# Performance work log

Hardware: AMD Instinct MI355X
Metric: run time of the kernel (lower is better)

## Reference

```python
import jax, jax.numpy as jnp
import numpy as np

NBINS = 29
NODES = 5


def setup_inputs() -> dict:
    key = jax.random.key(0)
    ks = jax.random.split(key, 9)
    B, Tq, Td, V, H = 64, 32, 4096, 100000, 300
    sentence = jax.random.randint(ks[0], (B, Td), 0, V)
    query_sentence = jax.random.randint(ks[1], (B, Tq), 0, V)
    query_idf = jax.random.uniform(ks[2], (B, Tq), jnp.float32)
    emb = jax.random.normal(ks[3], (V, H), jnp.float32)
    w1 = jax.random.uniform(ks[4], (NBINS + 1, NODES), jnp.float32, -0.1, 0.1)
    b1 = jnp.zeros((NODES,), jnp.float32)
    w2 = jax.random.uniform(ks[5], (NODES, 1), jnp.float32, -0.1, 0.1)
    b2 = jnp.zeros((1,), jnp.float32)
    gate_w = jax.random.uniform(ks[6], (1,), jnp.float32, -0.01, 0.01)
    out_w = jax.random.normal(ks[7], (1, 1), jnp.float32) * 0.1
    out_b = jnp.zeros((1,), jnp.float32)
    return dict(sentence=sentence, query_sentence=query_sentence, query_idf=query_idf,
                emb=emb, w1=w1, b1=b1, w2=w2, b2=b2, gate_w=gate_w, out_w=out_w, out_b=out_b)


def reference(sentence, query_sentence, query_idf, emb, w1, b1, w2, b2, gate_w, out_w, out_b):
    B, Td = sentence.shape
    Tq = query_sentence.shape[1]
    q_mask = (query_sentence != 0).astype(jnp.float32)  # (B,Tq)
    d_mask = (sentence != 0).astype(jnp.float32)        # (B,Td)
    qx = emb[query_sentence]                            # (B,Tq,H)
    dx = emb[sentence]                                  # (B,Td,H)
    q_norm = jnp.sqrt(jnp.sum(qx * qx, -1) + 1e-7)[:, :, None] + 1e-7
    d_norm = jnp.sqrt(jnp.sum(dx * dx, -1) + 1e-7)[:, None, :] + 1e-7
    sim = jnp.einsum('bqh,bdh->bqd', qx, dx) / q_norm / d_norm  # (B,Tq,Td)
    sim = sim + (1.0 - d_mask)[:, None, :] * 1e7  # push masked doc positions out of all bins
    # Histogram: original does nbins cumulative (sim < ub) passes then a cumulative
    # subtraction; equivalent per-element bin index + one scatter-add pass.
    ubs = jnp.linspace(-1.0, 1.0, NBINS + 1)[1:]
    idx = jnp.searchsorted(ubs, sim, side='right')  # bin j <=> ub[j-1] <= sim < ub[j]; NBINS = out-of-range
    rows = jnp.arange(B * Tq)[:, None]
    counts = jnp.zeros((B * Tq, NBINS), jnp.float32).at[rows, idx.reshape(B * Tq, Td)].add(1.0, mode='drop')
    counts = counts.reshape(B, Tq, NBINS)
    exact = jnp.sum((sim > 0.999) & (sim < 1.001), axis=-1).astype(jnp.float32)  # exact-match bin
    hist = jnp.log(jnp.concatenate([counts, exact[..., None]], axis=-1) + 1.0)   # histType == 'LCH'
    ffw = jnp.tanh(jnp.tanh(hist @ w1 + b1) @ w2 + b2)[..., 0]  # (B,Tq)
    # gateType == 'IDF': Linear(1,1,bias=False) on idf, masked softmax over query terms
    gate_logits = query_idf * gate_w[0] + (1.0 - q_mask) * -1e7
    w = jax.nn.softmax(gate_logits, axis=1)
    x = jnp.sum(w * ffw, axis=-1, keepdims=True)  # (B,1)
    return x * out_w[0, 0] + out_b
```

## Files before the change

kernel.cpp:

```cpp
#include <hip/hip_runtime.h>
#include <hip/hip_bf16.h>
#include <math.h>

#define B_    64
#define TQ    32
#define TD    4096
#define HDIM  300
#define NB    29
#define NFEAT 30
#define NKT   19
#define THREADS 256
#define NCH   2
#define DPB   128
#define RDEP  8
#define QF_SLOTS (NKT * 2 * 64)
#define QF_F4    (QF_SLOTS / 2)
#define QF_BYTES (QF_SLOTS * 8)

typedef _Float16 half4 __attribute__((ext_vector_type(4)));
typedef float    f32x4 __attribute__((ext_vector_type(4)));

__device__ __forceinline__ float ubf(int k) {
    return (float)(-1.0 + (2.0 * (double)(k + 1)) / 29.0);
}

__device__ __forceinline__ void bin_one(float sim, unsigned* s_hist, int q) {
    if (sim > 0.999f && sim < 1.001f) {
        atomicAdd(&s_hist[q * NFEAT + 28], 1u);
        atomicAdd(&s_hist[q * NFEAT + 29], 1u);
    } else {
        int idx = (int)((sim + 1.0f) * 14.5f);
        idx = idx < 0 ? 0 : (idx > NB ? NB : idx);
        while (idx < NB && sim >= ubf(idx)) ++idx;
        while (idx > 0 && sim < ubf(idx - 1)) --idx;
        if (idx < NB) atomicAdd(&s_hist[q * NFEAT + idx], 1u);
    }
}

__global__ void k_qfrag(const int* __restrict__ qsent, const float* __restrict__ emb,
                        _Float16* __restrict__ qf, float* __restrict__ invq,
                        unsigned* __restrict__ ghist) {
    const int b = blockIdx.x;
    const int t = threadIdx.x;
    const int row = t & 31, seg = t >> 5;
    __shared__ float pn[8][TQ];
    for (int i = t; i < TQ * NFEAT; i += 256) ghist[b * TQ * NFEAT + i] = 0u;
    const int tok = qsent[b * TQ + row];
    const float* p = emb + (size_t)tok * HDIM;
    _Float16* qfb = qf + (size_t)b * (QF_SLOTS * 4);
    float n = 0.f;
#pragma unroll
    for (int i = 0; i < 10; ++i) {
        const int jf = seg * 10 + i;
        if (jf < 76) {
            const int kg = jf * 4;
            float4 v = make_float4(0.f, 0.f, 0.f, 0.f);
            if (kg < 297) v = *(const float4*)(p + kg);
            n = fmaf(v.x, v.x, n); n = fmaf(v.y, v.y, n);
            n = fmaf(v.z, v.z, n); n = fmaf(v.w, v.w, n);
            half4 h = {(_Float16)v.x, (_Float16)v.y, (_Float16)v.z, (_Float16)v.w};
            const int kt = jf >> 2, g = jf & 3;
            const int slot = (kt * 2 + (row >> 4)) * 64 + (row & 15) + 16 * g;
            *(half4*)&qfb[slot * 4] = h;
        }
    }
    pn[seg][row] = n;
    __syncthreads();
    if (t < TQ) {
        float s = ((pn[0][t] + pn[1][t]) + (pn[2][t] + pn[3][t]))
                + ((pn[4][t] + pn[5][t]) + (pn[6][t] + pn[7][t]));
        invq[b * TQ + t] = 1.0f / (sqrtf(s + 1e-7f) + 1e-7f);
    }
}

__global__ __launch_bounds__(THREADS) void k_main(
        const int* __restrict__ sent, const float* __restrict__ emb,
        const _Float16* __restrict__ qf, const float* __restrict__ invq,
        unsigned* __restrict__ ghist) {
    __shared__ __align__(16) _Float16 afr[QF_SLOTS * 4];
    __shared__ float    s_iq[TQ];
    __shared__ unsigned s_hist[TQ * NFEAT];

    const int b    = blockIdx.x >> 5;
    const int d0   = (blockIdx.x & 31) * DPB;
    const int tid  = threadIdx.x;
    const int wid  = tid >> 6;
    const int lane = tid & 63;

    const int g4   = lane >> 4;
    const int r16  = lane & 15;

    int tok[NCH];
    const float* bp[NCH];
#pragma unroll
    for (int ch = 0; ch < NCH; ++ch) {
        tok[ch] = sent[b * TD + d0 + ch * 64 + wid * 16 + r16];
        bp[ch]  = emb + (size_t)tok[ch] * HDIM + g4 * 4;
    }

    auto ldBg = [&](int g) -> float4 {
        const int ch = g / NKT, kt = g - ch * NKT;
        if (kt == 18 && g4 == 3) return make_float4(0.f, 0.f, 0.f, 0.f);
        return *(const float4*)(bp[ch] + kt * 16);
    };

    float4 pre[RDEP];
#pragma unroll
    for (int p = 0; p < RDEP; ++p) pre[p] = ldBg(p);

    for (int i = tid; i < TQ * NFEAT; i += THREADS) s_hist[i] = 0u;
    {
        const float4* qfp = (const float4*)(qf + (size_t)b * (QF_SLOTS * 4));
        float4* afp = (float4*)afr;
        for (int i = tid; i < QF_F4; i += THREADS) afp[i] = qfp[i];
    }
    if (tid < TQ) s_iq[tid] = invq[b * TQ + tid];
    __syncthreads();

#pragma unroll
    for (int ch = 0; ch < NCH; ++ch) {
        f32x4 acc0 = {0.f, 0.f, 0.f, 0.f};
        f32x4 acc1 = {0.f, 0.f, 0.f, 0.f};
        float nd = 0.f;
#pragma unroll
        for (int kt = 0; kt < NKT; ++kt) {
            const int g = ch * NKT + kt;
            float4 v = pre[g % RDEP];
            if (g + RDEP < NCH * NKT) pre[g % RDEP] = ldBg(g + RDEP);
            nd = fmaf(v.x, v.x, nd); nd = fmaf(v.y, v.y, nd);
            nd = fmaf(v.z, v.z, nd); nd = fmaf(v.w, v.w, nd);
            half4 hb = {(_Float16)v.x, (_Float16)v.y, (_Float16)v.z, (_Float16)v.w};
            half4 a0 = *(const half4*)&afr[((kt * 2 + 0) * 64 + lane) * 4];
            half4 a1 = *(const half4*)&afr[((kt * 2 + 1) * 64 + lane) * 4];
            acc0 = __builtin_amdgcn_mfma_f32_16x16x16f16(a0, hb, acc0, 0, 0, 0);
            acc1 = __builtin_amdgcn_mfma_f32_16x16x16f16(a1, hb, acc1, 0, 0, 0);
        }
        float t = nd;
        t += __shfl_xor(t, 16, 64);
        t += __shfl_xor(t, 32, 64);
        const float idv = 1.0f / (sqrtf(t + 1e-7f) + 1e-7f);
        if (tok[ch] != 0) {
#pragma unroll
            for (int r = 0; r < 4; ++r) {
                const int q0 = g4 * 4 + r;
                bin_one(acc0[r] * s_iq[q0] * idv, s_hist, q0);
                const int q1 = 16 + g4 * 4 + r;
                bin_one(acc1[r] * s_iq[q1] * idv, s_hist, q1);
            }
        }
    }
    __syncthreads();
    for (int i = tid; i < TQ * NFEAT; i += THREADS) {
        unsigned v = s_hist[i];
        if (v) atomicAdd(&ghist[b * TQ * NFEAT + i], v);
    }
}

__global__ void k_finish(const unsigned* __restrict__ ghist,
                         const int* __restrict__ qsent, const float* __restrict__ idf,
                         const float* __restrict__ w1, const float* __restrict__ b1,
                         const float* __restrict__ w2, const float* __restrict__ b2,
                         const float* __restrict__ gw, const float* __restrict__ ow,
                         const float* __restrict__ ob, float* __restrict__ out) {
    int b = blockIdx.x;
    int lane = threadIdx.x;
    float ffw = 0.f;
    float logit = -3.0e38f;
    if (lane < TQ) {
        const unsigned* h = ghist + (b * TQ + lane) * NFEAT;
        float f[NFEAT];
        for (int k = 0; k < NFEAT; ++k) f[k] = logf((float)h[k] + 1.0f);
        float s2 = b2[0];
        for (int n = 0; n < 5; ++n) {
            float s = b1[n];
            for (int k = 0; k < NFEAT; ++k) s = fmaf(f[k], w1[k * 5 + n], s);
            s2 = fmaf(tanhf(s), w2[n], s2);
        }
        ffw = tanhf(s2);
        int qt = qsent[b * TQ + lane];
        logit = idf[b * TQ + lane] * gw[0] + (qt == 0 ? -1e7f : 0.f);
    }
    float m = logit;
#pragma unroll
    for (int t = 1; t < 64; t <<= 1) m = fmaxf(m, __shfl_xor(m, t, 64));
    float e = expf(logit - m);
    float se = e, sw = e * ffw;
#pragma unroll
    for (int t = 1; t < 64; t <<= 1) {
        se += __shfl_xor(se, t, 64);
        sw += __shfl_xor(sw, t, 64);
    }
    if (lane == 0) out[b] = (sw / se) * ow[0] + ob[0];
}

extern "C" void kernel_launch(void* const* d_in, const int* in_sizes, int n_in,
                              void* d_out, int out_size, void* d_ws, size_t ws_size,
                              hipStream_t stream) {
    const int*   sent  = (const int*)d_in[0];
    const int*   qsent = (const int*)d_in[1];
    const float* idf   = (const float*)d_in[2];
    const float* emb   = (const float*)d_in[3];
    const float* w1    = (const float*)d_in[4];
    const float* b1    = (const float*)d_in[5];
    const float* w2    = (const float*)d_in[6];
    const float* b2    = (const float*)d_in[7];
    const float* gw    = (const float*)d_in[8];
    const float* ow    = (const float*)d_in[9];
    const float* ob    = (const float*)d_in[10];
    float* out = (float*)d_out;

    char* ws = (char*)d_ws;
    unsigned*  ghist = (unsigned*)ws;
    _Float16*  qfrag = (_Float16*)(ws + (256 << 10));
    float*     invq  = (float*)(ws + (256 << 10) + (size_t)B_ * QF_BYTES);

    k_qfrag<<<B_, 256, 0, stream>>>(qsent, emb, qfrag, invq, ghist);
    k_main<<<B_ * (TD / DPB), THREADS, 0, stream>>>(sent, emb, qfrag, invq, ghist);
    k_finish<<<B_, 64, 0, stream>>>(ghist, qsent, idf, w1, b1, w2, b2, gw, ow, ob, out);
}
```

Baseline: 82.89 us.

## Bucket-sort document tokens by vocab id before gathering embeddings

Adds a per-batch counting-sort kernel that groups each row's document tokens into 1024 buckets by token id (id>>7). The main kernel then reads tokens in that order, so nearby threads and blocks gather embedding rows from nearby memory, which should improve cache and TLB locality. The histogram is order-independent, so results stay the same. The cost is an extra kernel launch plus a global write and read of the sorted token array, and bucket boundaries assume token ids below 131072.

```diff
diff --git a/kernel.cpp b/kernel.cpp
--- a/kernel.cpp
+++ b/kernel.cpp
@@ -13,6 +13,7 @@
 #define NCH   2
 #define DPB   128
 #define RDEP  8
+#define NBUCK 1024
 #define QF_SLOTS (NKT * 2 * 64)
 #define QF_F4    (QF_SLOTS / 2)
 #define QF_BYTES (QF_SLOTS * 8)
@@ -34,6 +35,46 @@
         while (idx < NB && sim >= ubf(idx)) ++idx;
         while (idx > 0 && sim < ubf(idx - 1)) --idx;
         if (idx < NB) atomicAdd(&s_hist[q * NFEAT + idx], 1u);
+    }
+}
+
+__global__ void k_sort(const int* __restrict__ sent, int* __restrict__ sorted) {
+    const int b = blockIdx.x;
+    const int t = threadIdx.x;
+    const int lane = t & 63, wv = t >> 6;
+    __shared__ unsigned cnt[NBUCK];
+    __shared__ unsigned wtot[4];
+    for (int i = t; i < NBUCK; i += 256) cnt[i] = 0u;
+    __syncthreads();
+    int tk[16];
+#pragma unroll
+    for (int j = 0; j < 16; ++j) tk[j] = sent[b * TD + j * 256 + t];
+#pragma unroll
+    for (int j = 0; j < 16; ++j) atomicAdd(&cnt[(unsigned)tk[j] >> 7], 1u);
+    __syncthreads();
+    unsigned c0 = cnt[t * 4], c1 = cnt[t * 4 + 1], c2 = cnt[t * 4 + 2], c3 = cnt[t * 4 + 3];
+    unsigned s = c0 + c1 + c2 + c3;
+    unsigned v = s;
+#pragma unroll
+    for (int d = 1; d < 64; d <<= 1) {
+        unsigned n = __shfl_up(v, d, 64);
+        if (lane >= d) v += n;
+    }
+    if (lane == 63) wtot[wv] = v;
+    __syncthreads();
+    unsigned wbase = 0;
+    for (int w = 0; w < wv; ++w) wbase += wtot[w];
+    const unsigned base = wbase + v - s;
+    __syncthreads();
+    cnt[t * 4]     = base;
+    cnt[t * 4 + 1] = base + c0;
+    cnt[t * 4 + 2] = base + c0 + c1;
+    cnt[t * 4 + 3] = base + c0 + c1 + c2;
+    __syncthreads();
+#pragma unroll
+    for (int j = 0; j < 16; ++j) {
+        unsigned pos = atomicAdd(&cnt[(unsigned)tk[j] >> 7], 1u);
+        sorted[b * TD + pos] = tk[j];
     }
 }
 
@@ -74,7 +115,7 @@
 }
 
 __global__ __launch_bounds__(THREADS) void k_main(
-        const int* __restrict__ sent, const float* __restrict__ emb,
+        const int* __restrict__ sorted, const float* __restrict__ emb,
         const _Float16* __restrict__ qf, const float* __restrict__ invq,
         unsigned* __restrict__ ghist) {
     __shared__ __align__(16) _Float16 afr[QF_SLOTS * 4];
@@ -94,7 +135,7 @@
     const float* bp[NCH];
 #pragma unroll
     for (int ch = 0; ch < NCH; ++ch) {
-        tok[ch] = sent[b * TD + d0 + ch * 64 + wid * 16 + r16];
+        tok[ch] = sorted[b * TD + d0 + ch * 64 + wid * 16 + r16];
         bp[ch]  = emb + (size_t)tok[ch] * HDIM + g4 * 4;
     }
 
@@ -210,11 +251,14 @@
     float* out = (float*)d_out;
 
     char* ws = (char*)d_ws;
-    unsigned*  ghist = (unsigned*)ws;
-    _Float16*  qfrag = (_Float16*)(ws + (256 << 10));
-    float*     invq  = (float*)(ws + (256 << 10) + (size_t)B_ * QF_BYTES);
-
+    unsigned*  ghist  = (unsigned*)ws;
+    _Float16*  qfrag  = (_Float16*)(ws + (256 << 10));
+    float*     invq   = (float*)(ws + (256 << 10) + (size_t)B_ * QF_BYTES);
+    int*       sorted = (int*)(ws + (256 << 10) + (size_t)B_ * QF_BYTES
+                               + (size_t)B_ * TQ * 4);
+
+    k_sort<<<B_, 256, 0, stream>>>(sent, sorted);
     k_qfrag<<<B_, 256, 0, stream>>>(qsent, emb, qfrag, invq, ghist);
-    k_main<<<B_ * (TD / DPB), THREADS, 0, stream>>>(sent, emb, qfrag, invq, ghist);
+    k_main<<<B_ * (TD / DPB), THREADS, 0, stream>>>(sorted, emb, qfrag, invq, ghist);
     k_finish<<<B_, 64, 0, stream>>>(ghist, qsent, idf, w1, b1, w2, b2, gw, ow, ob, out);
 }
```

Result: faster. 80.76 us (-2.6%).
